# Optimization experiments

Measured on AMD Instinct MI355X. Metric: run time of the kernel, lower is better.

## Reference

```python
import jax, jax.numpy as jnp
import numpy as np

P, S, IMG = 8, 4, 256          # patch_size, stride, img_size
HID, GH, B = 64, 128, 4        # conv hidden ch, gcn hidden ch, batch
Ph = (IMG - P) // S + 1        # 63 patches per side
N = Ph * Ph                    # 3969 patch-nodes


def _conv(x, w, b):
    y = jax.lax.conv_general_dilated(x, w, (1, 1), 'SAME',
                                     dimension_numbers=('NCHW', 'OIHW', 'NCHW'))
    return y + b[None, :, None, None]


def _img2patch(x):
    # x: [B,1,H,W] -> [B, N, P*P] (row-major patch pixels, matching torch reshape)
    pt = jax.lax.conv_general_dilated_patches(x, (P, P), (S, S), 'VALID')  # [B, P*P, Ph, Pw]
    b = x.shape[0]
    return pt.reshape(b, P * P, N).transpose(0, 2, 1)


def _patch2img(y):
    # y: [b, N, P*P] -> [b, 1, IMG, IMG] via overlap scatter-add
    b = y.shape[0]
    y = y.reshape(b, Ph, Ph, P, P)
    x = jnp.zeros((b, 1, IMG, IMG), y.dtype)
    hi = S * (Ph - 1) + 1
    for i in range(P):          # fixed small loop over patch pixels (64 iters)
        for j in range(P):
            x = x.at[:, 0, i:i + hi:S, j:j + hi:S].add(y[:, :, :, i, j])
    return x


def _gcn(x, adj, w, bias):
    # x: [B,N,F_in], adj: [B,N,N] -> [B,N,F_out]
    support = jnp.einsum('bnf,fg->bng', x, w)
    return jnp.einsum('bnm,bmg->bng', adj, support) + bias


def setup_inputs() -> dict:
    key = jax.random.key(0)
    ks = jax.random.split(key, 14)
    sc = 0.05
    return {
        'input_data': jax.random.normal(ks[0], (B, 1, IMG, IMG), jnp.float32),
        'proj': jax.random.normal(ks[1], (B, 1, IMG, IMG), jnp.float32),
        'adj': jax.random.uniform(ks[2], (B, N, N), jnp.float32) / N,
        'lam': jnp.float32(0.5),
        'conv_w1': jax.random.normal(ks[3], (HID, 1, 3, 3), jnp.float32) * sc,
        'conv_b1': jnp.zeros((HID,), jnp.float32),
        'conv_w2': jax.random.normal(ks[4], (HID, HID, 3, 3), jnp.float32) * sc,
        'conv_b2': jnp.zeros((HID,), jnp.float32),
        'conv_w3': jax.random.normal(ks[5], (1, HID, 3, 3), jnp.float32) * sc,
        'conv_b3': jnp.zeros((1,), jnp.float32),
        'gcn_w3': jax.random.normal(ks[6], (P * P, GH), jnp.float32) * sc,
        'gcn_b3': jnp.zeros((GH,), jnp.float32),
        'gcn_w4': jax.random.normal(ks[7], (GH, P * P), jnp.float32) * sc,
        'gcn_b4': jnp.zeros((P * P,), jnp.float32),
    }


def reference(input_data, proj, adj, lam,
              conv_w1, conv_b1, conv_w2, conv_b2, conv_w3, conv_b3,
              gcn_w3, gcn_b3, gcn_w4, gcn_b4):
    # block1: data-fidelity step (fidelity_module modeled as DC update)
    tmp1 = input_data + lam * (proj - input_data)
    # block2: 3-layer CNN
    h = jax.nn.relu(_conv(input_data, conv_w1, conv_b1))
    h = jax.nn.relu(_conv(h, conv_w2, conv_b2))
    tmp2 = _conv(h, conv_w3, conv_b3)
    # block3/4: patch-graph GCN branch
    patch = _img2patch(input_data)                 # [B, N, P*P]
    g = jax.nn.relu(_gcn(patch, adj, gcn_w3, gcn_b3))
    g = _gcn(g, adj, gcn_w4, gcn_b4)               # [B, N, P*P]
    # Patch2Im with overlap-count normalization mask
    mask = _patch2img(jnp.ones((1, N, P * P), jnp.float32))
    tmp3 = _patch2img(g) / mask
    return jax.nn.relu(tmp1 + tmp2 + tmp3)
```

## Files before the change

kernel.cpp:

```cpp
#include <hip/hip_runtime.h>

#define IMG   256
#define NPIX  65536
#define PH    63
#define NNODE 3969
#define SN    4000
#define HID   64
#define GH    128
#define BATCH 4

typedef __attribute__((ext_vector_type(8))) short short8;
typedef __attribute__((ext_vector_type(4))) float float4v;
typedef unsigned short ushort_t;

__device__ inline ushort_t f2bf(float f) {
    union { float f; unsigned u; } v; v.f = f;
    unsigned r = v.u + 0x7FFF + ((v.u >> 16) & 1);
    return (ushort_t)(r >> 16);
}

__global__ __launch_bounds__(256) void k_cvt_adj(const float* __restrict__ adj,
                                                 ushort_t* __restrict__ adjb) {
    int n = blockIdx.x, b = blockIdx.y;
    const float* src = adj + (size_t)(b * NNODE + n) * NNODE;
    unsigned* dst = (unsigned*)(adjb + (size_t)(b * NNODE + n) * SN);
    for (int c2 = threadIdx.x; c2 < SN / 2; c2 += 256) {
        int c = c2 * 2;
        float f0 = (c < NNODE) ? src[c] : 0.f;
        float f1 = (c + 1 < NNODE) ? src[c + 1] : 0.f;
        dst[c2] = (unsigned)f2bf(f0) | ((unsigned)f2bf(f1) << 16);
    }
}

__global__ __launch_bounds__(256) void k_sup1(const float* __restrict__ in,
                                              const float* __restrict__ w3,
                                              ushort_t* __restrict__ sup1T) {
    int b = blockIdx.z;
    int g = blockIdx.y * 8 + (threadIdx.x >> 5);
    int n = blockIdx.x * 32 + (threadIdx.x & 31);
    ushort_t* dst = sup1T + (size_t)b * GH * SN + (size_t)g * SN + n;
    if (n >= NNODE) { *dst = 0; return; }
    int py = n / PH, px = n - py * PH;
    const float* base = in + (size_t)b * NPIX + (py * 4) * IMG + px * 4;
    float acc = 0.f;
#pragma unroll
    for (int i = 0; i < 8; ++i)
#pragma unroll
        for (int j = 0; j < 8; ++j)
            acc += base[i * IMG + j] * w3[(i * 8 + j) * GH + g];
    *dst = f2bf(acc);
}

template <int G>
__global__ __launch_bounds__(256) void k_gemm_mfma(const ushort_t* __restrict__ adjb,
                                                   const ushort_t* __restrict__ supT,
                                                   float* __restrict__ C) {
    constexpr int FN = (G == 128) ? 4 : 2;
    const int b = blockIdx.z, ks = blockIdx.y;
    const int node0 = blockIdx.x * 128;
    const int t = threadIdx.x;
    const int lane = t & 63, w = t >> 6;
    const int l15 = lane & 15, q = lane >> 4;
    const int wm0 = (G == 128) ? (w & 1) * 64 : 0;
    const int wn0 = (G == 128) ? (w >> 1) * 64 : w * 32;

    __shared__ ushort_t Als[G][72];
    __shared__ ushort_t Bls[128][72];

    const int k0c = ks * 992;
    const int kend = (ks == 3) ? NNODE : k0c + 992;
    const int kiters = (kend - k0c + 31) >> 5;
    const int npairs = (kiters + 1) >> 1;

    const ushort_t* Ab = supT + (size_t)b * G * SN;
    const ushort_t* Bb = adjb + (size_t)b * NNODE * SN;
    float* Cb = C + (size_t)b * G * SN;

    float4v acc[4][FN];
#pragma unroll
    for (int i = 0; i < 4; ++i)
#pragma unroll
        for (int j = 0; j < FN; ++j)
#pragma unroll
            for (int r = 0; r < 4; ++r) acc[i][j][r] = 0.f;

    for (int kp = 0; kp < npairs; ++kp) {
        const int kb0 = k0c + kp * 64;
        const bool has2 = (kp * 2 + 1 < kiters);
#pragma unroll
        for (int i = 0; i < G / 64; ++i) {
            int idx = t + i * 256;
            int r = idx >> 2, s = idx & 3;
            *(uint4*)&Als[r][s * 8] =
                *(const uint4*)&Ab[(size_t)r * SN + kb0 + s * 8];
        }
#pragma unroll
        for (int i = 0; i < 2; ++i) {
            int idx = t + i * 256;
            int r = idx >> 2, s = idx & 3;
            *(uint4*)&Bls[r][s * 8] =
                *(const uint4*)&Bb[(size_t)(node0 + r) * SN + kb0 + s * 8];
        }
        if (has2) {
#pragma unroll
            for (int i = 0; i < G / 64; ++i) {
                int idx = t + i * 256;
                int r = idx >> 2, s = idx & 3;
                *(uint4*)&Als[r][32 + s * 8] =
                    *(const uint4*)&Ab[(size_t)r * SN + kb0 + 32 + s * 8];
            }
#pragma unroll
            for (int i = 0; i < 2; ++i) {
                int idx = t + i * 256;
                int r = idx >> 2, s = idx & 3;
                *(uint4*)&Bls[r][32 + s * 8] =
                    *(const uint4*)&Bb[(size_t)(node0 + r) * SN + kb0 + 32 + s * 8];
            }
        }
        __syncthreads();
        {
            short8 af[4], bf[FN];
#pragma unroll
            for (int i = 0; i < 4; ++i)
                af[i] = *(const short8*)&Als[wm0 + i * 16 + l15][q * 8];
#pragma unroll
            for (int j = 0; j < FN; ++j)
                bf[j] = *(const short8*)&Bls[wn0 + j * 16 + l15][q * 8];
#pragma unroll
            for (int i = 0; i < 4; ++i)
#pragma unroll
                for (int j = 0; j < FN; ++j)
                    acc[i][j] = __builtin_amdgcn_mfma_f32_16x16x32_bf16(
                        af[i], bf[j], acc[i][j], 0, 0, 0);
        }
        if (has2) {
            short8 af[4], bf[FN];
#pragma unroll
            for (int i = 0; i < 4; ++i)
                af[i] = *(const short8*)&Als[wm0 + i * 16 + l15][32 + q * 8];
#pragma unroll
            for (int j = 0; j < FN; ++j)
                bf[j] = *(const short8*)&Bls[wn0 + j * 16 + l15][32 + q * 8];
#pragma unroll
            for (int i = 0; i < 4; ++i)
#pragma unroll
                for (int j = 0; j < FN; ++j)
                    acc[i][j] = __builtin_amdgcn_mfma_f32_16x16x32_bf16(
                        af[i], bf[j], acc[i][j], 0, 0, 0);
        }
        __syncthreads();
    }
#pragma unroll
    for (int i = 0; i < 4; ++i) {
        int gg = wm0 + i * 16 + q * 4;
#pragma unroll
        for (int j = 0; j < FN; ++j) {
            int nn = node0 + wn0 + j * 16 + l15;
            if (nn < NNODE) {
#pragma unroll
                for (int r = 0; r < 4; ++r)
                    unsafeAtomicAdd(&Cb[(size_t)(gg + r) * SN + nn], acc[i][j][r]);
            }
        }
    }
}

__global__ __launch_bounds__(256) void k_sup2(const float* __restrict__ g1T,
                                              const float* __restrict__ gb3,
                                              const float* __restrict__ w4,
                                              ushort_t* __restrict__ sup2T) {
    int b = blockIdx.z;
    int g = blockIdx.y * 8 + (threadIdx.x >> 5);
    int n = blockIdx.x * 32 + (threadIdx.x & 31);
    const float* gb = g1T + (size_t)b * GH * SN + n;
    float acc = 0.f;
#pragma unroll 8
    for (int k = 0; k < GH; ++k) {
        float v = fmaxf(gb[(size_t)k * SN] + gb3[k], 0.f);
        acc += v * w4[k * 64 + g];
    }
    sup2T[(size_t)b * 64 * SN + (size_t)g * SN + n] = (n < NNODE) ? f2bf(acc) : 0;
}

__global__ __launch_bounds__(256) void k_prepack(const float* __restrict__ w,
                                                 ushort_t* __restrict__ W2p) {
    int idx = blockIdx.x * 256 + threadIdx.x;
    if (idx >= 36864) return;
    int tap = idx >> 12, rem = idx & 4095;
    int oc = rem >> 6, ic = rem & 63;
    W2p[idx] = f2bf(w[(oc * 64 + ic) * 9 + tap]);
}

__global__ __launch_bounds__(256) void k_conv2f(const float* __restrict__ in,
                                                const float* __restrict__ w1,
                                                const float* __restrict__ b1,
                                                const ushort_t* __restrict__ W2p,
                                                const float* __restrict__ b2,
                                                const float* __restrict__ w3c,
                                                float* __restrict__ U) {
    __shared__ ushort_t Xs[340 * 72];
    __shared__ float pre[1088];
    const int b = blockIdx.z;
    const float* inb = in + (size_t)b * NPIX;
    float* Uball = U + (size_t)b * 9 * NPIX;
    const int t = threadIdx.x;
    const int lane = t & 63, w = t >> 6;
    const int l15 = lane & 15, q = lane >> 4;
    const int x0 = blockIdx.x * 32, y0 = blockIdx.y * 8;

    float* sI  = pre;
    float* ws1 = pre + 432;
    float* bs1 = pre + 1008;

    for (int idx = t; idx < 432; idx += 256) {
        int yy = idx / 36, xx = idx - yy * 36;
        int gy = y0 + yy - 2, gx = x0 + xx - 2;
        sI[idx] = (gy >= 0 && gy < IMG && gx >= 0 && gx < IMG) ? inb[gy * IMG + gx] : 0.f;
    }
    for (int idx = t; idx < 576; idx += 256) ws1[idx] = w1[idx];
    if (t < 64) bs1[t] = b1[t];
    __syncthreads();

    for (int idx = t; idx < 2720; idx += 256) {
        int hp = idx >> 3, s = idx & 7;
        int hy = hp / 34, hx = hp - hy * 34;
        int gy = y0 + hy - 1, gx = x0 + hx - 1;
        unsigned pk[4] = {0u, 0u, 0u, 0u};
        if (gy >= 0 && gy < IMG && gx >= 0 && gx < IMG) {
            float r[9];
#pragma unroll
            for (int dy = 0; dy < 3; ++dy)
#pragma unroll
                for (int dx = 0; dx < 3; ++dx)
                    r[dy * 3 + dx] = sI[(hy + dy) * 36 + hx + dx];
#pragma unroll
            for (int h = 0; h < 4; ++h) {
                int oc0 = s * 8 + h * 2;
                float a0 = bs1[oc0], a1 = bs1[oc0 + 1];
#pragma unroll
                for (int k = 0; k < 9; ++k) {
                    a0 += r[k] * ws1[oc0 * 9 + k];
                    a1 += r[k] * ws1[(oc0 + 1) * 9 + k];
                }
                a0 = fmaxf(a0, 0.f); a1 = fmaxf(a1, 0.f);
                pk[h] = (unsigned)f2bf(a0) | ((unsigned)f2bf(a1) << 16);
            }
        }
        *(uint4*)&Xs[hp * 72 + s * 8] = *(uint4*)pk;
    }
    __syncthreads();

    for (int idx = t; idx < 576; idx += 256) pre[idx] = w3c[idx];

    const int wn0 = w * 64;
    int pbase[4];
#pragma unroll
    for (int j = 0; j < 4; ++j) {
        int p = wn0 + j * 16 + l15;
        pbase[j] = (p >> 5) * 34 + (p & 31);
    }

    float4v acc[4][4];
#pragma unroll
    for (int i = 0; i < 4; ++i)
#pragma unroll
        for (int j = 0; j < 4; ++j)
#pragma unroll
            for (int r = 0; r < 4; ++r) acc[i][j][r] = 0.f;

    for (int tap = 0; tap < 9; ++tap) {
        int ky = tap / 3, kx = tap - ky * 3;
        const ushort_t* wp = W2p + tap * 4096;
#pragma unroll
        for (int c = 0; c < 2; ++c) {
            short8 af[4], bf[4];
#pragma unroll
            for (int i = 0; i < 4; ++i)
                af[i] = *(const short8*)&wp[(i * 16 + l15) * 64 + c * 32 + q * 8];
#pragma unroll
            for (int j = 0; j < 4; ++j)
                bf[j] = *(const short8*)&Xs[(pbase[j] + ky * 34 + kx) * 72 + c * 32 + q * 8];
#pragma unroll
            for (int i = 0; i < 4; ++i)
#pragma unroll
                for (int j = 0; j < 4; ++j)
                    acc[i][j] = __builtin_amdgcn_mfma_f32_16x16x32_bf16(
                        af[i], bf[j], acc[i][j], 0, 0, 0);
        }
    }
    __syncthreads();

    float b2r[16];
#pragma unroll
    for (int i = 0; i < 4; ++i)
#pragma unroll
        for (int r = 0; r < 4; ++r) b2r[i * 4 + r] = b2[i * 16 + q * 4 + r];

#pragma unroll
    for (int j = 0; j < 4; ++j) {
        float u[9];
#pragma unroll
        for (int d = 0; d < 9; ++d) u[d] = 0.f;
#pragma unroll
        for (int i = 0; i < 4; ++i)
#pragma unroll
            for (int r = 0; r < 4; ++r) {
                int oc = i * 16 + q * 4 + r;
                float h = fmaxf(acc[i][j][r] + b2r[i * 4 + r], 0.f);
#pragma unroll
                for (int d = 0; d < 9; ++d) u[d] += h * pre[oc * 9 + d];
            }
#pragma unroll
        for (int d = 0; d < 9; ++d) {
            u[d] += __shfl_xor(u[d], 16, 64);
            u[d] += __shfl_xor(u[d], 32, 64);
        }
        int p = wn0 + j * 16 + l15;
        int y = y0 + (p >> 5), x = x0 + (p & 31);
#pragma unroll
        for (int dd = 0; dd < 3; ++dd) {
            int d = q + dd * 4;
            if (d < 9)
                Uball[(size_t)d * NPIX + (size_t)y * IMG + x] = u[d];
        }
    }
}

__global__ __launch_bounds__(256) void k_combine(const float* __restrict__ in,
                                                 const float* __restrict__ proj,
                                                 const float* __restrict__ lamp,
                                                 const float* __restrict__ U,
                                                 const float* __restrict__ bc,
                                                 const float* __restrict__ g2T,
                                                 const float* __restrict__ gb4,
                                                 float* __restrict__ out) {
    int b = blockIdx.z;
    const float* inb = in + (size_t)b * NPIX;
    const float* prb = proj + (size_t)b * NPIX;
    const float* Ub = U + (size_t)b * 9 * NPIX;
    const float* g2b = g2T + (size_t)b * 64 * SN;
    int tx = threadIdx.x & 15, ty = threadIdx.x >> 4;
    int x = blockIdx.x * 16 + tx, y = blockIdx.y * 16 + ty;

    float acc = bc[0];
#pragma unroll
    for (int dy = 0; dy < 3; ++dy) {
        int yy = y + dy - 1;
#pragma unroll
        for (int dx = 0; dx < 3; ++dx) {
            int xx = x + dx - 1;
            if (yy >= 0 && yy < IMG && xx >= 0 && xx < IMG)
                acc += Ub[(size_t)(dy * 3 + dx) * NPIX + (size_t)yy * IMG + xx];
        }
    }

    float iv = inb[y * IMG + x], pv = prb[y * IMG + x];
    float tmp1 = iv + lamp[0] * (pv - iv);

    int pylo = (y >= 4) ? ((y - 4) >> 2) : 0;
    int pyhi = min(62, y >> 2);
    int pxlo = (x >= 4) ? ((x - 4) >> 2) : 0;
    int pxhi = min(62, x >> 2);
    float sum = 0.f;
    int cnt = 0;
    for (int py = pylo; py <= pyhi; ++py)
        for (int px = pxlo; px <= pxhi; ++px) {
            int pix = (y - 4 * py) * 8 + (x - 4 * px);
            sum += g2b[(size_t)pix * SN + (py * PH + px)] + gb4[pix];
            ++cnt;
        }
    float tmp3 = sum / (float)cnt;

    out[(size_t)b * NPIX + y * IMG + x] = fmaxf(tmp1 + acc + tmp3, 0.f);
}

extern "C" void kernel_launch(void* const* d_in, const int* in_sizes, int n_in,
                              void* d_out, int out_size, void* d_ws, size_t ws_size,
                              hipStream_t stream) {
    const float* input = (const float*)d_in[0];
    const float* proj  = (const float*)d_in[1];
    const float* adj   = (const float*)d_in[2];
    const float* lam   = (const float*)d_in[3];
    const float* cw1   = (const float*)d_in[4];
    const float* cb1   = (const float*)d_in[5];
    const float* cw2   = (const float*)d_in[6];
    const float* cb2   = (const float*)d_in[7];
    const float* cw3   = (const float*)d_in[8];
    const float* cb3   = (const float*)d_in[9];
    const float* gw3   = (const float*)d_in[10];
    const float* gb3   = (const float*)d_in[11];
    const float* gw4   = (const float*)d_in[12];
    const float* gb4   = (const float*)d_in[13];
    float* out = (float*)d_out;

    char* base = (char*)d_ws;
    float*    g2T   = (float*)base;
    char*     pool  = base + 4096000;
    ushort_t* adjb  = (ushort_t*)pool;
    ushort_t* sup1T = (ushort_t*)(pool + 127008000);
    float*    g1T   = (float*)(pool + 127008000 + 4096000);
    ushort_t* sup2T = (ushort_t*)(pool + 127008000 + 4096000 + 8192000);
    float*    U     = (float*)pool;
    ushort_t* W2p   = (ushort_t*)(pool + 9437184);

    dim3 blk(256);

    hipMemsetAsync(g1T, 0, 8192000, stream);
    hipMemsetAsync(g2T, 0, 4096000, stream);

    k_cvt_adj<<<dim3(NNODE, BATCH), blk, 0, stream>>>(adj, adjb);
    k_sup1<<<dim3(125, 16, BATCH), blk, 0, stream>>>(input, gw3, sup1T);
    k_gemm_mfma<128><<<dim3(32, 4, BATCH), blk, 0, stream>>>(adjb, sup1T, g1T);
    k_sup2<<<dim3(125, 8, BATCH), blk, 0, stream>>>(g1T, gb3, gw4, sup2T);
    k_gemm_mfma<64><<<dim3(32, 4, BATCH), blk, 0, stream>>>(adjb, sup2T, g2T);

    k_prepack<<<dim3(144), blk, 0, stream>>>(cw2, W2p);
    k_conv2f<<<dim3(8, 32, BATCH), blk, 0, stream>>>(input, cw1, cb1, W2p, cb2, cw3, U);
    k_combine<<<dim3(16, 16, BATCH), blk, 0, stream>>>(
        input, proj, lam, U, cb3, g2T, gb4, out);
}
```

Measured before the change: 669.0 us.

## Fuse fp32-to-bf16 adjacency conversion into first GCN GEMM

Removes the separate adjacency conversion kernel and makes the first MFMA GEMM read fp32 adj directly, converting to bf16 while staging into shared memory and writing the bf16 copy out for the second GEMM. This saves one full extra read of the bf16 adjacency and a kernel launch. The trade-off is that the GEMM's staging loads now use scalar fp32 reads with conversion inside the main loop, which may lengthen the critical path, and the grid has only 512 blocks to carry that bandwidth.

```diff
diff --git a/kernel.cpp b/kernel.cpp
--- a/kernel.cpp
+++ b/kernel.cpp
@@ -17,19 +17,6 @@
     union { float f; unsigned u; } v; v.f = f;
     unsigned r = v.u + 0x7FFF + ((v.u >> 16) & 1);
     return (ushort_t)(r >> 16);
-}
-
-__global__ __launch_bounds__(256) void k_cvt_adj(const float* __restrict__ adj,
-                                                 ushort_t* __restrict__ adjb) {
-    int n = blockIdx.x, b = blockIdx.y;
-    const float* src = adj + (size_t)(b * NNODE + n) * NNODE;
-    unsigned* dst = (unsigned*)(adjb + (size_t)(b * NNODE + n) * SN);
-    for (int c2 = threadIdx.x; c2 < SN / 2; c2 += 256) {
-        int c = c2 * 2;
-        float f0 = (c < NNODE) ? src[c] : 0.f;
-        float f1 = (c + 1 < NNODE) ? src[c + 1] : 0.f;
-        dst[c2] = (unsigned)f2bf(f0) | ((unsigned)f2bf(f1) << 16);
-    }
 }
 
 __global__ __launch_bounds__(256) void k_sup1(const float* __restrict__ in,
@@ -49,6 +36,137 @@
         for (int j = 0; j < 8; ++j)
             acc += base[i * IMG + j] * w3[(i * 8 + j) * GH + g];
     *dst = f2bf(acc);
+}
+
+__global__ __launch_bounds__(256) void k_gemm_cvt128(const float* __restrict__ adj,
+                                                     ushort_t* __restrict__ adjb,
+                                                     const ushort_t* __restrict__ supT,
+                                                     float* __restrict__ C) {
+    const int b = blockIdx.z, ks = blockIdx.y;
+    const int node0 = blockIdx.x * 128;
+    const int t = threadIdx.x;
+    const int lane = t & 63, w = t >> 6;
+    const int l15 = lane & 15, q = lane >> 4;
+    const int wm0 = (w & 1) * 64;
+    const int wn0 = (w >> 1) * 64;
+
+    __shared__ ushort_t Als[128][72];
+    __shared__ ushort_t Bls[128][72];
+
+    const int k0c = ks * 992;
+    const int kend = (ks == 3) ? NNODE : k0c + 992;
+    const int kiters = (kend - k0c + 31) >> 5;
+    const int npairs = (kiters + 1) >> 1;
+
+    const ushort_t* Ab = supT + (size_t)b * 128 * SN;
+    const float*    Aj = adj  + (size_t)b * NNODE * NNODE;
+    ushort_t*       Jb = adjb + (size_t)b * NNODE * SN;
+    float* Cb = C + (size_t)b * 128 * SN;
+
+    float4v acc[4][4];
+#pragma unroll
+    for (int i = 0; i < 4; ++i)
+#pragma unroll
+        for (int j = 0; j < 4; ++j)
+#pragma unroll
+            for (int r = 0; r < 4; ++r) acc[i][j][r] = 0.f;
+
+    auto stageB = [&](int kb, int loff) {
+#pragma unroll
+        for (int i = 0; i < 2; ++i) {
+            int idx = t + i * 256;
+            int r = idx >> 2, s = idx & 3;
+            int row = node0 + r;
+            int col = kb + s * 8;
+            unsigned pk[4] = {0u, 0u, 0u, 0u};
+            if (row < NNODE) {
+                const float* src = Aj + (size_t)row * NNODE + col;
+                if (col + 8 <= NNODE) {
+#pragma unroll
+                    for (int h = 0; h < 4; ++h)
+                        pk[h] = (unsigned)f2bf(src[2 * h]) |
+                                ((unsigned)f2bf(src[2 * h + 1]) << 16);
+                } else {
+#pragma unroll
+                    for (int h = 0; h < 4; ++h) {
+                        float f0 = (col + 2 * h     < NNODE) ? src[2 * h]     : 0.f;
+                        float f1 = (col + 2 * h + 1 < NNODE) ? src[2 * h + 1] : 0.f;
+                        pk[h] = (unsigned)f2bf(f0) | ((unsigned)f2bf(f1) << 16);
+                    }
+                }
+                *(uint4*)&Jb[(size_t)row * SN + col] = *(uint4*)pk;
+            }
+            *(uint4*)&Bls[r][loff + s * 8] = *(uint4*)pk;
+        }
+    };
+
+    for (int kp = 0; kp < npairs; ++kp) {
+        const int kb0 = k0c + kp * 64;
+        const bool has2 = (kp * 2 + 1 < kiters);
+#pragma unroll
+        for (int i = 0; i < 2; ++i) {
+            int idx = t + i * 256;
+            int r = idx >> 2, s = idx & 3;
+            *(uint4*)&Als[r][s * 8] =
+                *(const uint4*)&Ab[(size_t)r * SN + kb0 + s * 8];
+        }
+        if (has2) {
+#pragma unroll
+            for (int i = 0; i < 2; ++i) {
+                int idx = t + i * 256;
+                int r = idx >> 2, s = idx & 3;
+                *(uint4*)&Als[r][32 + s * 8] =
+                    *(const uint4*)&Ab[(size_t)r * SN + kb0 + 32 + s * 8];
+            }
+        }
+        stageB(kb0, 0);
+        if (has2) stageB(kb0 + 32, 32);
+        __syncthreads();
+        {
+            short8 af[4], bf[4];
+#pragma unroll
+            for (int i = 0; i < 4; ++i)
+                af[i] = *(const short8*)&Als[wm0 + i * 16 + l15][q * 8];
+#pragma unroll
+            for (int j = 0; j < 4; ++j)
+                bf[j] = *(const short8*)&Bls[wn0 + j * 16 + l15][q * 8];
+#pragma unroll
+            for (int i = 0; i < 4; ++i)
+#pragma unroll
+                for (int j = 0; j < 4; ++j)
+                    acc[i][j] = __builtin_amdgcn_mfma_f32_16x16x32_bf16(
+                        af[i], bf[j], acc[i][j], 0, 0, 0);
+        }
+        if (has2) {
+            short8 af[4], bf[4];
+#pragma unroll
+            for (int i = 0; i < 4; ++i)
+                af[i] = *(const short8*)&Als[wm0 + i * 16 + l15][32 + q * 8];
+#pragma unroll
+            for (int j = 0; j < 4; ++j)
+                bf[j] = *(const short8*)&Bls[wn0 + j * 16 + l15][32 + q * 8];
+#pragma unroll
+            for (int i = 0; i < 4; ++i)
+#pragma unroll
+                for (int j = 0; j < 4; ++j)
+                    acc[i][j] = __builtin_amdgcn_mfma_f32_16x16x32_bf16(
+                        af[i], bf[j], acc[i][j], 0, 0, 0);
+        }
+        __syncthreads();
+    }
+#pragma unroll
+    for (int i = 0; i < 4; ++i) {
+        int gg = wm0 + i * 16 + q * 4;
+#pragma unroll
+        for (int j = 0; j < 4; ++j) {
+            int nn = node0 + wn0 + j * 16 + l15;
+            if (nn < NNODE) {
+#pragma unroll
+                for (int r = 0; r < 4; ++r)
+                    unsafeAtomicAdd(&Cb[(size_t)(gg + r) * SN + nn], acc[i][j][r]);
+            }
+        }
+    }
 }
 
 template <int G>
@@ -408,9 +526,8 @@
     hipMemsetAsync(g1T, 0, 8192000, stream);
     hipMemsetAsync(g2T, 0, 4096000, stream);
 
-    k_cvt_adj<<<dim3(NNODE, BATCH), blk, 0, stream>>>(adj, adjb);
     k_sup1<<<dim3(125, 16, BATCH), blk, 0, stream>>>(input, gw3, sup1T);
-    k_gemm_mfma<128><<<dim3(32, 4, BATCH), blk, 0, stream>>>(adjb, sup1T, g1T);
+    k_gemm_cvt128<<<dim3(32, 4, BATCH), blk, 0, stream>>>(adj, adjb, sup1T, g1T);
     k_sup2<<<dim3(125, 8, BATCH), blk, 0, stream>>>(g1T, gb3, gw4, sup2T);
     k_gemm_mfma<64><<<dim3(32, 4, BATCH), blk, 0, stream>>>(adjb, sup2T, g2T);
 
```

New measurement: 672.3 us. About the same (+0.5%).

## Fuse adjacency fp32-to-bf16 conversion into GEMM tile loads and double split-K

Applied to the files above, without the earlier changes.

Removes the standalone kernel that converted the full adjacency matrix to a padded bf16 copy. Both GCN GEMMs now read fp32 adjacency directly and round it to bf16 while staging tiles into shared memory. This avoids writing and re-reading the intermediate bf16 copy. The trade-off is that each GEMM streams the fp32 matrix, twice the bytes of the bf16 copy, using scalar rather than 128-bit loads. The K split also goes from 4 to 8 slices, which launches more blocks but adds more partial-sum accumulation into the outputs.

```diff
diff --git a/kernel.cpp b/kernel.cpp
--- a/kernel.cpp
+++ b/kernel.cpp
@@ -17,19 +17,6 @@
     union { float f; unsigned u; } v; v.f = f;
     unsigned r = v.u + 0x7FFF + ((v.u >> 16) & 1);
     return (ushort_t)(r >> 16);
-}
-
-__global__ __launch_bounds__(256) void k_cvt_adj(const float* __restrict__ adj,
-                                                 ushort_t* __restrict__ adjb) {
-    int n = blockIdx.x, b = blockIdx.y;
-    const float* src = adj + (size_t)(b * NNODE + n) * NNODE;
-    unsigned* dst = (unsigned*)(adjb + (size_t)(b * NNODE + n) * SN);
-    for (int c2 = threadIdx.x; c2 < SN / 2; c2 += 256) {
-        int c = c2 * 2;
-        float f0 = (c < NNODE) ? src[c] : 0.f;
-        float f1 = (c + 1 < NNODE) ? src[c + 1] : 0.f;
-        dst[c2] = (unsigned)f2bf(f0) | ((unsigned)f2bf(f1) << 16);
-    }
 }
 
 __global__ __launch_bounds__(256) void k_sup1(const float* __restrict__ in,
@@ -52,9 +39,9 @@
 }
 
 template <int G>
-__global__ __launch_bounds__(256) void k_gemm_mfma(const ushort_t* __restrict__ adjb,
-                                                   const ushort_t* __restrict__ supT,
-                                                   float* __restrict__ C) {
+__global__ __launch_bounds__(256) void k_gemm_cvt(const float* __restrict__ adj,
+                                                  const ushort_t* __restrict__ supT,
+                                                  float* __restrict__ C) {
     constexpr int FN = (G == 128) ? 4 : 2;
     const int b = blockIdx.z, ks = blockIdx.y;
     const int node0 = blockIdx.x * 128;
@@ -67,14 +54,17 @@
     __shared__ ushort_t Als[G][72];
     __shared__ ushort_t Bls[128][72];
 
-    const int k0c = ks * 992;
-    const int kend = (ks == 3) ? NNODE : k0c + 992;
+    const int k0c = ks * 512;
+    const int kend = (k0c + 512 < NNODE) ? (k0c + 512) : NNODE;
     const int kiters = (kend - k0c + 31) >> 5;
     const int npairs = (kiters + 1) >> 1;
 
     const ushort_t* Ab = supT + (size_t)b * G * SN;
-    const ushort_t* Bb = adjb + (size_t)b * NNODE * SN;
+    const float*    Aj = adj  + (size_t)b * NNODE * NNODE;
     float* Cb = C + (size_t)b * G * SN;
+
+    const int brow = t >> 5;
+    const int bcol = t & 31;
 
     float4v acc[4][FN];
 #pragma unroll
@@ -93,13 +83,6 @@
             int r = idx >> 2, s = idx & 3;
             *(uint4*)&Als[r][s * 8] =
                 *(const uint4*)&Ab[(size_t)r * SN + kb0 + s * 8];
-        }
-#pragma unroll
-        for (int i = 0; i < 2; ++i) {
-            int idx = t + i * 256;
-            int r = idx >> 2, s = idx & 3;
-            *(uint4*)&Bls[r][s * 8] =
-                *(const uint4*)&Bb[(size_t)(node0 + r) * SN + kb0 + s * 8];
         }
         if (has2) {
 #pragma unroll
@@ -109,12 +92,22 @@
                 *(uint4*)&Als[r][32 + s * 8] =
                     *(const uint4*)&Ab[(size_t)r * SN + kb0 + 32 + s * 8];
             }
-#pragma unroll
-            for (int i = 0; i < 2; ++i) {
-                int idx = t + i * 256;
-                int r = idx >> 2, s = idx & 3;
-                *(uint4*)&Bls[r][32 + s * 8] =
-                    *(const uint4*)&Bb[(size_t)(node0 + r) * SN + kb0 + 32 + s * 8];
+        }
+        {
+            const bool cok0 = (kb0 + bcol) < NNODE;
+            const bool cok1 = (kb0 + 32 + bcol) < NNODE;
+#pragma unroll
+            for (int i = 0; i < 16; ++i) {
+                int row = brow + i * 8;
+                int grow = node0 + row;
+                bool rok = grow < NNODE;
+                const float* src = Aj + (size_t)grow * NNODE;
+                float v0 = (rok && cok0) ? src[kb0 + bcol] : 0.f;
+                Bls[row][bcol] = f2bf(v0);
+                if (has2) {
+                    float v1 = (rok && cok1) ? src[kb0 + 32 + bcol] : 0.f;
+                    Bls[row][32 + bcol] = f2bf(v1);
+                }
             }
         }
         __syncthreads();
@@ -396,10 +389,9 @@
     char* base = (char*)d_ws;
     float*    g2T   = (float*)base;
     char*     pool  = base + 4096000;
-    ushort_t* adjb  = (ushort_t*)pool;
-    ushort_t* sup1T = (ushort_t*)(pool + 127008000);
-    float*    g1T   = (float*)(pool + 127008000 + 4096000);
-    ushort_t* sup2T = (ushort_t*)(pool + 127008000 + 4096000 + 8192000);
+    ushort_t* sup1T = (ushort_t*)pool;
+    float*    g1T   = (float*)(pool + 4096000);
+    ushort_t* sup2T = (ushort_t*)(pool + 4096000 + 8192000);
     float*    U     = (float*)pool;
     ushort_t* W2p   = (ushort_t*)(pool + 9437184);
 
@@ -408,11 +400,10 @@
     hipMemsetAsync(g1T, 0, 8192000, stream);
     hipMemsetAsync(g2T, 0, 4096000, stream);
 
-    k_cvt_adj<<<dim3(NNODE, BATCH), blk, 0, stream>>>(adj, adjb);
     k_sup1<<<dim3(125, 16, BATCH), blk, 0, stream>>>(input, gw3, sup1T);
-    k_gemm_mfma<128><<<dim3(32, 4, BATCH), blk, 0, stream>>>(adjb, sup1T, g1T);
+    k_gemm_cvt<128><<<dim3(32, 8, BATCH), blk, 0, stream>>>(adj, sup1T, g1T);
     k_sup2<<<dim3(125, 8, BATCH), blk, 0, stream>>>(g1T, gb3, gw4, sup2T);
-    k_gemm_mfma<64><<<dim3(32, 4, BATCH), blk, 0, stream>>>(adjb, sup2T, g2T);
+    k_gemm_cvt<64><<<dim3(32, 8, BATCH), blk, 0, stream>>>(adj, sup2T, g2T);
 
     k_prepack<<<dim3(144), blk, 0, stream>>>(cw2, W2p);
     k_conv2f<<<dim3(8, 32, BATCH), blk, 0, stream>>>(input, cw1, cb1, W2p, cb2, cw3, U);
```

Result: slower. 992.0 us (+48.3%).
